# Kernel tuning notes

Measured on AMD Instinct MI355X. Metric: run time of the kernel, lower is better.

## Reference

```python
import jax, jax.numpy as jnp
import numpy as np

N = 50000
E = 800000
IN_CH = 256
HID = 32
HEADS = 4
OUT_CH = 40
NEG_SLOPE = 0.2
BN_EPS = 1e-5


def _gat_conv(x, W, att_src, att_dst, bias, src, dst, num_nodes, concat):
    # x: [N, F_in]; W: [F_in, H*C]; att_src/att_dst: [H, C]
    H, C = att_src.shape
    h = (x @ W).reshape(num_nodes, H, C)            # [N, H, C]
    a_src = (h * att_src[None]).sum(-1)             # [N, H]
    a_dst = (h * att_dst[None]).sum(-1)             # [N, H]
    e = jax.nn.leaky_relu(a_src[src] + a_dst[dst], NEG_SLOPE)  # [Etot, H]
    # segment softmax over incoming edges of each destination node
    m = jax.ops.segment_max(e, dst, num_segments=num_nodes)    # [N, H]
    ex = jnp.exp(e - m[dst])
    s = jax.ops.segment_sum(ex, dst, num_segments=num_nodes)   # [N, H]
    alpha = ex / (s[dst] + 1e-16)                   # [Etot, H]
    out = jax.ops.segment_sum(h[src] * alpha[:, :, None], dst,
                              num_segments=num_nodes)          # [N, H, C]
    out = out.reshape(num_nodes, H * C) if concat else out.mean(axis=1)
    return out + bias


def setup_inputs() -> dict:
    key = jax.random.key(0)
    ks = jax.random.split(key, 12)
    x = jax.random.normal(ks[0], (N, IN_CH), dtype=jnp.float32)
    edge_index = jax.random.randint(ks[1], (2, E), 0, N, dtype=jnp.int64)
    # layer 1: in -> heads*hid, concat
    W1 = jax.random.normal(ks[2], (IN_CH, HEADS * HID), dtype=jnp.float32) * (1.0 / np.sqrt(IN_CH))
    att_src1 = jax.random.normal(ks[3], (HEADS, HID), dtype=jnp.float32) * 0.1
    att_dst1 = jax.random.normal(ks[4], (HEADS, HID), dtype=jnp.float32) * 0.1
    b1 = jnp.zeros((HEADS * HID,), dtype=jnp.float32)
    # batch norm over hidden*heads features
    gamma = jnp.ones((HEADS * HID,), dtype=jnp.float32)
    beta = jnp.zeros((HEADS * HID,), dtype=jnp.float32)
    # layer 2: heads*hid -> out, heads=1, mean (concat=False)
    W2 = jax.random.normal(ks[5], (HEADS * HID, OUT_CH), dtype=jnp.float32) * (1.0 / np.sqrt(HEADS * HID))
    att_src2 = jax.random.normal(ks[6], (1, OUT_CH), dtype=jnp.float32) * 0.1
    att_dst2 = jax.random.normal(ks[7], (1, OUT_CH), dtype=jnp.float32) * 0.1
    b2 = jnp.zeros((OUT_CH,), dtype=jnp.float32)
    return {"x": x, "edge_index": edge_index, "W1": W1, "att_src1": att_src1,
            "att_dst1": att_dst1, "b1": b1, "gamma": gamma, "beta": beta,
            "W2": W2, "att_src2": att_src2, "att_dst2": att_dst2, "b2": b2}


def reference(x, edge_index, W1, att_src1, att_dst1, b1, gamma, beta,
              W2, att_src2, att_dst2, b2):
    num_nodes = x.shape[0]
    loops = jnp.arange(num_nodes, dtype=edge_index.dtype)
    src = jnp.concatenate([edge_index[0], loops])   # add self-loops (PyG default)
    dst = jnp.concatenate([edge_index[1], loops])
    h = _gat_conv(x, W1, att_src1, att_dst1, b1, src, dst, num_nodes, concat=True)
    # BatchNorm over nodes (training-mode batch statistics)
    mu = h.mean(axis=0)
    var = h.var(axis=0)
    h = (h - mu) * jax.lax.rsqrt(var + BN_EPS) * gamma + beta
    h = jax.nn.elu(h)
    out = _gat_conv(h, W2, att_src2, att_dst2, b2, src, dst, num_nodes, concat=False)
    return out
```

## Files before the change

### kernel.cpp

```cpp
#include <hip/hip_runtime.h>

#define NN 50000
#define EE 800000
#define ETOT 850000
#define FIN 256
#define F1 128
#define F2 40
#define CAP 48
#define G1B ((NN + 127) / 128)
#define FILLB ((EE / 4 + NN + 255) / 256)
#define PB ((NN + 63) / 64)

typedef unsigned int u32;
typedef unsigned short u16;

static __device__ __forceinline__ u32 f2bf(float f) {
  u32 u = __float_as_uint(f);
  return (u + 0x7FFFu + ((u >> 16) & 1u)) >> 16;
}
#define BF_LO(u) __uint_as_float((u) << 16)
#define BF_HI(u) __uint_as_float((u) & 0xFFFF0000u)

__global__ __launch_bounds__(256) void g1f_kernel(const float* __restrict__ x,
                                                  const float* __restrict__ W1,
                                                  const float* __restrict__ att_src,
                                                  const float* __restrict__ att_dst,
                                                  u32* __restrict__ h1bf,
                                                  float* __restrict__ a_src,
                                                  float* __restrict__ a_dst,
                                                  const int* __restrict__ ei,
                                                  int* __restrict__ cnt,
                                                  int* __restrict__ csr) {
  __shared__ float Alds[16 * 132];
  __shared__ float Blds[16 * 128];
  __shared__ float att_s[128], att_d[128];
  const int t = threadIdx.x;

  if (blockIdx.x >= G1B) {
    int i = (blockIdx.x - G1B) * 256 + t;
    if (i < EE / 4) {
      int e = i * 4;
      int4 s4 = *(const int4*)(ei + e);
      int4 d4 = *(const int4*)(ei + EE + e);
      int p0 = atomicAdd(cnt + d4.x, 1); if (p0 < CAP) csr[d4.x * CAP + p0] = s4.x;
      int p1 = atomicAdd(cnt + d4.y, 1); if (p1 < CAP) csr[d4.y * CAP + p1] = s4.y;
      int p2 = atomicAdd(cnt + d4.z, 1); if (p2 < CAP) csr[d4.z * CAP + p2] = s4.z;
      int p3 = atomicAdd(cnt + d4.w, 1); if (p3 < CAP) csr[d4.w * CAP + p3] = s4.w;
    } else {
      int n = i - EE / 4;
      if (n < NN) {
        int p = atomicAdd(cnt + n, 1);
        if (p < CAP) csr[n * CAP + p] = n;
      }
    }
    return;
  }

  if (t < 128) { att_s[t] = att_src[t]; att_d[t] = att_dst[t]; }
  const int m0 = blockIdx.x * 128;
  const int arow = t >> 1;
  const int akk = (t & 1) * 8;
  const int brow = t >> 4;
  const int bc = (t & 15) * 8;
  const int ty = t >> 4;
  const int tx = t & 15;

  float acc[8][8];
#pragma unroll
  for (int i = 0; i < 8; ++i)
#pragma unroll
    for (int j = 0; j < 8; ++j) acc[i][j] = 0.f;

  for (int k0 = 0; k0 < FIN; k0 += 16) {
    float4 a0 = {0.f, 0.f, 0.f, 0.f}, a1 = {0.f, 0.f, 0.f, 0.f};
    int gr = m0 + arow;
    if (gr < NN) {
      a0 = *(const float4*)(x + (size_t)gr * FIN + k0 + akk);
      a1 = *(const float4*)(x + (size_t)gr * FIN + k0 + akk + 4);
    }
    float4 b0 = *(const float4*)(W1 + (size_t)(k0 + brow) * F1 + bc);
    float4 b1 = *(const float4*)(W1 + (size_t)(k0 + brow) * F1 + bc + 4);
    __syncthreads();
    Alds[(akk + 0) * 132 + arow] = a0.x;
    Alds[(akk + 1) * 132 + arow] = a0.y;
    Alds[(akk + 2) * 132 + arow] = a0.z;
    Alds[(akk + 3) * 132 + arow] = a0.w;
    Alds[(akk + 4) * 132 + arow] = a1.x;
    Alds[(akk + 5) * 132 + arow] = a1.y;
    Alds[(akk + 6) * 132 + arow] = a1.z;
    Alds[(akk + 7) * 132 + arow] = a1.w;
    *(float4*)(Blds + brow * 128 + bc) = b0;
    *(float4*)(Blds + brow * 128 + bc + 4) = b1;
    __syncthreads();
#pragma unroll
    for (int k = 0; k < 16; ++k) {
      float4 av0 = *(const float4*)(Alds + k * 132 + ty * 8);
      float4 av1 = *(const float4*)(Alds + k * 132 + ty * 8 + 4);
      float4 bv0 = *(const float4*)(Blds + k * 128 + tx * 8);
      float4 bv1 = *(const float4*)(Blds + k * 128 + tx * 8 + 4);
      float aa[8] = {av0.x, av0.y, av0.z, av0.w, av1.x, av1.y, av1.z, av1.w};
      float bb[8] = {bv0.x, bv0.y, bv0.z, bv0.w, bv1.x, bv1.y, bv1.z, bv1.w};
#pragma unroll
      for (int i = 0; i < 8; ++i)
#pragma unroll
        for (int j = 0; j < 8; ++j) acc[i][j] = fmaf(aa[i], bb[j], acc[i][j]);
    }
  }
#pragma unroll
  for (int i = 0; i < 8; ++i) {
    int gr = m0 + ty * 8 + i;
    if (gr < NN) {
      uint4 w;
      w.x = f2bf(acc[i][0]) | (f2bf(acc[i][1]) << 16);
      w.y = f2bf(acc[i][2]) | (f2bf(acc[i][3]) << 16);
      w.z = f2bf(acc[i][4]) | (f2bf(acc[i][5]) << 16);
      w.w = f2bf(acc[i][6]) | (f2bf(acc[i][7]) << 16);
      *(uint4*)(h1bf + (size_t)gr * 64 + tx * 4) = w;
    }
  }
#pragma unroll
  for (int i = 0; i < 8; ++i) {
    float ps = 0.f, pd = 0.f;
#pragma unroll
    for (int j = 0; j < 8; ++j) {
      int c = tx * 8 + j;
      ps += acc[i][j] * att_s[c];
      pd += acc[i][j] * att_d[c];
    }
    ps += __shfl_xor(ps, 1); pd += __shfl_xor(pd, 1);
    ps += __shfl_xor(ps, 2); pd += __shfl_xor(pd, 2);
    if ((tx & 3) == 0) {
      int gr = m0 + ty * 8 + i;
      if (gr < NN) {
        int head = tx >> 2;
        a_src[gr * 4 + head] = ps;
        a_dst[gr * 4 + head] = pd;
      }
    }
  }
}

__global__ __launch_bounds__(256) void gather1_kernel(const int* __restrict__ cnt,
                                                      const int* __restrict__ csr,
                                                      const float* __restrict__ a_src,
                                                      const float* __restrict__ a_dst,
                                                      const u32* __restrict__ h1bf,
                                                      const float* __restrict__ b1,
                                                      float* __restrict__ h1b,
                                                      float* __restrict__ bnsum,
                                                      float* __restrict__ bnsq) {
  __shared__ float bns[32], bnq[32];
  int t = threadIdx.x;
  if (t < 32) { bns[t] = 0.f; bnq[t] = 0.f; }
  __syncthreads();
  int p = blockIdx.x / PB;
  int nb = blockIdx.x - p * PB;
  int n = nb * 64 + (t >> 2);
  int l = t & 3;
  int f0 = p * 32 + l * 8;
  if (n < NN) {
    float adst = a_dst[n * 4 + p];
    float acc[8] = {0.f, 0.f, 0.f, 0.f, 0.f, 0.f, 0.f, 0.f};
    float ssum = 0.f;
    const int* row = csr + n * CAP;
    int m = cnt[n]; if (m > CAP) m = CAP;
    const u32* hb = h1bf + p * 16 + l * 4;
    int i = 0;
    for (; i + 3 < m; i += 4) {
      int4 s4 = *(const int4*)(row + i);
      float e0 = a_src[s4.x * 4 + p] + adst;
      float e1 = a_src[s4.y * 4 + p] + adst;
      float e2 = a_src[s4.z * 4 + p] + adst;
      float e3 = a_src[s4.w * 4 + p] + adst;
      uint4 q0 = *(const uint4*)(hb + (size_t)s4.x * 64);
      uint4 q1 = *(const uint4*)(hb + (size_t)s4.y * 64);
      uint4 q2 = *(const uint4*)(hb + (size_t)s4.z * 64);
      uint4 q3 = *(const uint4*)(hb + (size_t)s4.w * 64);
      e0 = e0 > 0.f ? e0 : 0.2f * e0;  float x0 = __expf(e0);
      e1 = e1 > 0.f ? e1 : 0.2f * e1;  float x1 = __expf(e1);
      e2 = e2 > 0.f ? e2 : 0.2f * e2;  float x2 = __expf(e2);
      e3 = e3 > 0.f ? e3 : 0.2f * e3;  float x3 = __expf(e3);
      acc[0] = fmaf(x0, BF_LO(q0.x), acc[0]); acc[1] = fmaf(x0, BF_HI(q0.x), acc[1]);
      acc[2] = fmaf(x0, BF_LO(q0.y), acc[2]); acc[3] = fmaf(x0, BF_HI(q0.y), acc[3]);
      acc[4] = fmaf(x0, BF_LO(q0.z), acc[4]); acc[5] = fmaf(x0, BF_HI(q0.z), acc[5]);
      acc[6] = fmaf(x0, BF_LO(q0.w), acc[6]); acc[7] = fmaf(x0, BF_HI(q0.w), acc[7]);
      acc[0] = fmaf(x1, BF_LO(q1.x), acc[0]); acc[1] = fmaf(x1, BF_HI(q1.x), acc[1]);
      acc[2] = fmaf(x1, BF_LO(q1.y), acc[2]); acc[3] = fmaf(x1, BF_HI(q1.y), acc[3]);
      acc[4] = fmaf(x1, BF_LO(q1.z), acc[4]); acc[5] = fmaf(x1, BF_HI(q1.z), acc[5]);
      acc[6] = fmaf(x1, BF_LO(q1.w), acc[6]); acc[7] = fmaf(x1, BF_HI(q1.w), acc[7]);
      acc[0] = fmaf(x2, BF_LO(q2.x), acc[0]); acc[1] = fmaf(x2, BF_HI(q2.x), acc[1]);
      acc[2] = fmaf(x2, BF_LO(q2.y), acc[2]); acc[3] = fmaf(x2, BF_HI(q2.y), acc[3]);
      acc[4] = fmaf(x2, BF_LO(q2.z), acc[4]); acc[5] = fmaf(x2, BF_HI(q2.z), acc[5]);
      acc[6] = fmaf(x2, BF_LO(q2.w), acc[6]); acc[7] = fmaf(x2, BF_HI(q2.w), acc[7]);
      acc[0] = fmaf(x3, BF_LO(q3.x), acc[0]); acc[1] = fmaf(x3, BF_HI(q3.x), acc[1]);
      acc[2] = fmaf(x3, BF_LO(q3.y), acc[2]); acc[3] = fmaf(x3, BF_HI(q3.y), acc[3]);
      acc[4] = fmaf(x3, BF_LO(q3.z), acc[4]); acc[5] = fmaf(x3, BF_HI(q3.z), acc[5]);
      acc[6] = fmaf(x3, BF_LO(q3.w), acc[6]); acc[7] = fmaf(x3, BF_HI(q3.w), acc[7]);
      ssum += x0 + x1 + x2 + x3;
    }
    for (; i < m; ++i) {
      int s0 = row[i];
      float e0 = a_src[s0 * 4 + p] + adst;
      e0 = e0 > 0.f ? e0 : 0.2f * e0;
      float x0 = __expf(e0);
      uint4 q = *(const uint4*)(hb + (size_t)s0 * 64);
      acc[0] = fmaf(x0, BF_LO(q.x), acc[0]); acc[1] = fmaf(x0, BF_HI(q.x), acc[1]);
      acc[2] = fmaf(x0, BF_LO(q.y), acc[2]); acc[3] = fmaf(x0, BF_HI(q.y), acc[3]);
      acc[4] = fmaf(x0, BF_LO(q.z), acc[4]); acc[5] = fmaf(x0, BF_HI(q.z), acc[5]);
      acc[6] = fmaf(x0, BF_LO(q.w), acc[6]); acc[7] = fmaf(x0, BF_HI(q.w), acc[7]);
      ssum += x0;
    }
    float inv = 1.f / (ssum + 1e-16f);
    float4 b0 = *(const float4*)(b1 + f0);
    float4 b4 = *(const float4*)(b1 + f0 + 4);
    float o[8];
    o[0] = acc[0] * inv + b0.x; o[1] = acc[1] * inv + b0.y;
    o[2] = acc[2] * inv + b0.z; o[3] = acc[3] * inv + b0.w;
    o[4] = acc[4] * inv + b4.x; o[5] = acc[5] * inv + b4.y;
    o[6] = acc[6] * inv + b4.z; o[7] = acc[7] * inv + b4.w;
    float4 w0 = {o[0], o[1], o[2], o[3]};
    float4 w1 = {o[4], o[5], o[6], o[7]};
    *(float4*)(h1b + (size_t)n * F1 + f0) = w0;
    *(float4*)(h1b + (size_t)n * F1 + f0 + 4) = w1;
    int lb = l * 8;
#pragma unroll
    for (int j = 0; j < 8; ++j) {
      atomicAdd(&bns[lb + j], o[j]);
      atomicAdd(&bnq[lb + j], o[j] * o[j]);
    }
  }
  __syncthreads();
  if (t < 32) {
    atomicAdd(bnsum + p * 32 + t, bns[t]);
    atomicAdd(bnsq + p * 32 + t, bnq[t]);
  }
}

__global__ __launch_bounds__(256) void gemm2_kernel(const float* __restrict__ hpre,
                                                    const float* __restrict__ W2,
                                                    const float* __restrict__ bnsum,
                                                    const float* __restrict__ bnsq,
                                                    const float* __restrict__ gamma,
                                                    const float* __restrict__ beta,
                                                    const float* __restrict__ att_src2,
                                                    const float* __restrict__ att_dst2,
                                                    u16* __restrict__ h2bf,
                                                    float* __restrict__ a_src2,
                                                    float* __restrict__ a_dst2) {
  __shared__ float Wlds[128 * 40];
  __shared__ float Alds[16 * 128];
  __shared__ float sc[128], sh[128];
  int t = threadIdx.x;
  for (int i = t; i < 128 * 40; i += 256) Wlds[i] = W2[i];
  if (t < 128) {
    const float invN = 1.f / (float)NN;
    float mu = bnsum[t] * invN;
    float var = bnsq[t] * invN - mu * mu;
    float s = gamma[t] * rsqrtf(var + 1e-5f);
    sc[t] = s;
    sh[t] = beta[t] - mu * s;
  }
  int tr = t >> 3;
  int tc = t & 7;
  float as5[5], ad5[5];
#pragma unroll
  for (int j = 0; j < 5; ++j) { as5[j] = att_src2[tc * 5 + j]; ad5[j] = att_dst2[tc * 5 + j]; }
  int n0 = blockIdx.x * 128;
  int lrow = t >> 1;
  int lkk = (t & 1) * 8;
  float acc[4][5];
#pragma unroll
  for (int i = 0; i < 4; ++i)
#pragma unroll
    for (int j = 0; j < 5; ++j) acc[i][j] = 0.f;

  for (int k0 = 0; k0 < F1; k0 += 16) {
    float av[8];
    int gn = n0 + lrow;
    if (gn < NN) {
      float4 v0 = *(const float4*)(hpre + (size_t)gn * F1 + k0 + lkk);
      float4 v1 = *(const float4*)(hpre + (size_t)gn * F1 + k0 + lkk + 4);
      av[0] = v0.x; av[1] = v0.y; av[2] = v0.z; av[3] = v0.w;
      av[4] = v1.x; av[5] = v1.y; av[6] = v1.z; av[7] = v1.w;
    } else {
#pragma unroll
      for (int j = 0; j < 8; ++j) av[j] = 0.f;
    }
    __syncthreads();
#pragma unroll
    for (int j = 0; j < 8; ++j) {
      int kg = k0 + lkk + j;
      float a = av[j] * sc[kg] + sh[kg];
      a = a > 0.f ? a : (__expf(a) - 1.f);
      Alds[(lkk + j) * 128 + lrow] = a;
    }
    __syncthreads();
#pragma unroll
    for (int k = 0; k < 16; ++k) {
      float4 a4 = *(const float4*)(Alds + k * 128 + tr * 4);
      float aa[4] = {a4.x, a4.y, a4.z, a4.w};
      float w[5];
#pragma unroll
      for (int j = 0; j < 5; ++j) w[j] = Wlds[(k0 + k) * 40 + tc * 5 + j];
#pragma unroll
      for (int i = 0; i < 4; ++i)
#pragma unroll
        for (int j = 0; j < 5; ++j) acc[i][j] = fmaf(aa[i], w[j], acc[i][j]);
    }
  }
#pragma unroll
  for (int i = 0; i < 4; ++i) {
    int gn = n0 + tr * 4 + i;
    if (gn < NN) {
#pragma unroll
      for (int j = 0; j < 5; ++j)
        h2bf[(size_t)gn * 40 + tc * 5 + j] = (u16)f2bf(acc[i][j]);
    }
  }
#pragma unroll
  for (int i = 0; i < 4; ++i) {
    float ps = 0.f, pd = 0.f;
#pragma unroll
    for (int j = 0; j < 5; ++j) { ps += acc[i][j] * as5[j]; pd += acc[i][j] * ad5[j]; }
#pragma unroll
    for (int off = 1; off < 8; off <<= 1) {
      ps += __shfl_xor(ps, off);
      pd += __shfl_xor(pd, off);
    }
    if (tc == 0) {
      int gn = n0 + tr * 4 + i;
      if (gn < NN) { a_src2[gn] = ps; a_dst2[gn] = pd; }
    }
  }
}

__global__ __launch_bounds__(256) void gather2_kernel(const int* __restrict__ cnt,
                                                      const int* __restrict__ csr,
                                                      const float* __restrict__ a_src,
                                                      const float* __restrict__ a_dst,
                                                      const u32* __restrict__ h2bf,
                                                      const float* __restrict__ b2,
                                                      float* __restrict__ out) {
  int t = threadIdx.x;
  int n = blockIdx.x * 32 + (t >> 3);
  if (n >= NN) return;
  int l = t & 7;
  bool act = (l < 5);
  float adst = a_dst[n];
  float acc[8] = {0.f, 0.f, 0.f, 0.f, 0.f, 0.f, 0.f, 0.f};
  float ssum = 0.f;
  const int* row = csr + n * CAP;
  int m = cnt[n]; if (m > CAP) m = CAP;
  const uint4 zz = {0u, 0u, 0u, 0u};
  int i = 0;
  for (; i + 3 < m; i += 4) {
    int4 s4 = *(const int4*)(row + i);
    float e0 = a_src[s4.x] + adst;
    float e1 = a_src[s4.y] + adst;
    float e2 = a_src[s4.z] + adst;
    float e3 = a_src[s4.w] + adst;
    uint4 q0 = act ? *(const uint4*)(h2bf + (size_t)s4.x * 20 + l * 4) : zz;
    uint4 q1 = act ? *(const uint4*)(h2bf + (size_t)s4.y * 20 + l * 4) : zz;
    uint4 q2 = act ? *(const uint4*)(h2bf + (size_t)s4.z * 20 + l * 4) : zz;
    uint4 q3 = act ? *(const uint4*)(h2bf + (size_t)s4.w * 20 + l * 4) : zz;
    e0 = e0 > 0.f ? e0 : 0.2f * e0;  float x0 = __expf(e0);
    e1 = e1 > 0.f ? e1 : 0.2f * e1;  float x1 = __expf(e1);
    e2 = e2 > 0.f ? e2 : 0.2f * e2;  float x2 = __expf(e2);
    e3 = e3 > 0.f ? e3 : 0.2f * e3;  float x3 = __expf(e3);
    acc[0] = fmaf(x0, BF_LO(q0.x), acc[0]); acc[1] = fmaf(x0, BF_HI(q0.x), acc[1]);
    acc[2] = fmaf(x0, BF_LO(q0.y), acc[2]); acc[3] = fmaf(x0, BF_HI(q0.y), acc[3]);
    acc[4] = fmaf(x0, BF_LO(q0.z), acc[4]); acc[5] = fmaf(x0, BF_HI(q0.z), acc[5]);
    acc[6] = fmaf(x0, BF_LO(q0.w), acc[6]); acc[7] = fmaf(x0, BF_HI(q0.w), acc[7]);
    acc[0] = fmaf(x1, BF_LO(q1.x), acc[0]); acc[1] = fmaf(x1, BF_HI(q1.x), acc[1]);
    acc[2] = fmaf(x1, BF_LO(q1.y), acc[2]); acc[3] = fmaf(x1, BF_HI(q1.y), acc[3]);
    acc[4] = fmaf(x1, BF_LO(q1.z), acc[4]); acc[5] = fmaf(x1, BF_HI(q1.z), acc[5]);
    acc[6] = fmaf(x1, BF_LO(q1.w), acc[6]); acc[7] = fmaf(x1, BF_HI(q1.w), acc[7]);
    acc[0] = fmaf(x2, BF_LO(q2.x), acc[0]); acc[1] = fmaf(x2, BF_HI(q2.x), acc[1]);
    acc[2] = fmaf(x2, BF_LO(q2.y), acc[2]); acc[3] = fmaf(x2, BF_HI(q2.y), acc[3]);
    acc[4] = fmaf(x2, BF_LO(q2.z), acc[4]); acc[5] = fmaf(x2, BF_HI(q2.z), acc[5]);
    acc[6] = fmaf(x2, BF_LO(q2.w), acc[6]); acc[7] = fmaf(x2, BF_HI(q2.w), acc[7]);
    acc[0] = fmaf(x3, BF_LO(q3.x), acc[0]); acc[1] = fmaf(x3, BF_HI(q3.x), acc[1]);
    acc[2] = fmaf(x3, BF_LO(q3.y), acc[2]); acc[3] = fmaf(x3, BF_HI(q3.y), acc[3]);
    acc[4] = fmaf(x3, BF_LO(q3.z), acc[4]); acc[5] = fmaf(x3, BF_HI(q3.z), acc[5]);
    acc[6] = fmaf(x3, BF_LO(q3.w), acc[6]); acc[7] = fmaf(x3, BF_HI(q3.w), acc[7]);
    ssum += x0 + x1 + x2 + x3;
  }
  for (; i < m; ++i) {
    int s0 = row[i];
    float e0 = a_src[s0] + adst;
    e0 = e0 > 0.f ? e0 : 0.2f * e0;
    float x0 = __expf(e0);
    uint4 q = act ? *(const uint4*)(h2bf + (size_t)s0 * 20 + l * 4) : zz;
    acc[0] = fmaf(x0, BF_LO(q.x), acc[0]); acc[1] = fmaf(x0, BF_HI(q.x), acc[1]);
    acc[2] = fmaf(x0, BF_LO(q.y), acc[2]); acc[3] = fmaf(x0, BF_HI(q.y), acc[3]);
    acc[4] = fmaf(x0, BF_LO(q.z), acc[4]); acc[5] = fmaf(x0, BF_HI(q.z), acc[5]);
    acc[6] = fmaf(x0, BF_LO(q.w), acc[6]); acc[7] = fmaf(x0, BF_HI(q.w), acc[7]);
    ssum += x0;
  }
  float inv = 1.f / (ssum + 1e-16f);
  if (act) {
    float* op = out + (size_t)n * F2 + l * 8;
#pragma unroll
    for (int j = 0; j < 8; ++j) op[j] = acc[j] * inv + b2[l * 8 + j];
  }
}

extern "C" void kernel_launch(void* const* d_in, const int* in_sizes, int n_in,
                              void* d_out, int out_size, void* d_ws, size_t ws_size,
                              hipStream_t stream) {
  const float* x        = (const float*)d_in[0];
  const int*   ei       = (const int*)d_in[1];
  const float* W1       = (const float*)d_in[2];
  const float* att_src1 = (const float*)d_in[3];
  const float* att_dst1 = (const float*)d_in[4];
  const float* b1       = (const float*)d_in[5];
  const float* gamma    = (const float*)d_in[6];
  const float* beta     = (const float*)d_in[7];
  const float* W2       = (const float*)d_in[8];
  const float* att_src2 = (const float*)d_in[9];
  const float* att_dst2 = (const float*)d_in[10];
  const float* b2       = (const float*)d_in[11];
  float* out = (float*)d_out;

  int* cnt      = (int*)d_ws;
  float* bnsum  = (float*)(cnt + 50048);
  float* bnsq   = bnsum + 128;
  int* csr      = (int*)(bnsq + 128);
  u32* h1bf     = (u32*)(csr + NN * CAP);
  float* h1b    = (float*)(h1bf + 3200000);
  u32* h2bf     = (u32*)(h1b + 6400000);
  float* a_src1 = (float*)(h2bf + 1000000);
  float* a_dst1 = a_src1 + 200000;
  float* a_src2 = a_dst1 + 200000;
  float* a_dst2 = a_src2 + 50000;

  hipMemsetAsync(cnt, 0, (50048 + 256) * sizeof(int), stream);

  g1f_kernel<<<G1B + FILLB, 256, 0, stream>>>(x, W1, att_src1, att_dst1,
                                              h1bf, a_src1, a_dst1,
                                              ei, cnt, csr);
  gather1_kernel<<<4 * PB, 256, 0, stream>>>(cnt, csr, a_src1, a_dst1,
                                             h1bf, b1, h1b, bnsum, bnsq);
  gemm2_kernel<<<(NN + 127) / 128, 256, 0, stream>>>(h1b, W2, bnsum, bnsq,
                                                     gamma, beta,
                                                     att_src2, att_dst2,
                                                     (u16*)h2bf, a_src2, a_dst2);
  gather2_kernel<<<(NN + 31) / 32, 256, 0, stream>>>(cnt, csr, a_src2, a_dst2,
                                                     h2bf, b2, out);
}
```

Measured before the change: 323.8 us.

## Handle self-loops inline in gathers and split layer-2 features into aligned arrays

Self-loop edges are no longer written into the CSR by the fill blocks. Each gather kernel now adds the node's own contribution directly before walking its neighbour list, which removes N atomics and CSR writes and reads. The fill path goes back to one edge per thread with scalar loads instead of int4 vector loads. Layer-2 bf16 features, 80-byte rows before, are split into a 64-byte array and a 16-byte array so each gathered row is cache-line friendly, at the cost of two scattered loads per neighbour and a branchy store pattern in gemm2.

```diff
diff --git a/kernel.cpp b/kernel.cpp
--- a/kernel.cpp
+++ b/kernel.cpp
@@ -2,13 +2,12 @@
 
 #define NN 50000
 #define EE 800000
-#define ETOT 850000
 #define FIN 256
 #define F1 128
 #define F2 40
 #define CAP 48
 #define G1B ((NN + 127) / 128)
-#define FILLB ((EE / 4 + NN + 255) / 256)
+#define FILLB ((EE + 255) / 256)
 #define PB ((NN + 63) / 64)
 
 typedef unsigned int u32;
@@ -37,21 +36,12 @@
   const int t = threadIdx.x;
 
   if (blockIdx.x >= G1B) {
-    int i = (blockIdx.x - G1B) * 256 + t;
-    if (i < EE / 4) {
-      int e = i * 4;
-      int4 s4 = *(const int4*)(ei + e);
-      int4 d4 = *(const int4*)(ei + EE + e);
-      int p0 = atomicAdd(cnt + d4.x, 1); if (p0 < CAP) csr[d4.x * CAP + p0] = s4.x;
-      int p1 = atomicAdd(cnt + d4.y, 1); if (p1 < CAP) csr[d4.y * CAP + p1] = s4.y;
-      int p2 = atomicAdd(cnt + d4.z, 1); if (p2 < CAP) csr[d4.z * CAP + p2] = s4.z;
-      int p3 = atomicAdd(cnt + d4.w, 1); if (p3 < CAP) csr[d4.w * CAP + p3] = s4.w;
-    } else {
-      int n = i - EE / 4;
-      if (n < NN) {
-        int p = atomicAdd(cnt + n, 1);
-        if (p < CAP) csr[n * CAP + p] = n;
-      }
+    int e = (blockIdx.x - G1B) * 256 + t;
+    if (e < EE) {
+      int src = ei[e];
+      int dst = ei[EE + e];
+      int p = atomicAdd(cnt + dst, 1);
+      if (p < CAP) csr[dst * CAP + p] = src;
     }
     return;
   }
@@ -162,9 +152,20 @@
     float adst = a_dst[n * 4 + p];
     float acc[8] = {0.f, 0.f, 0.f, 0.f, 0.f, 0.f, 0.f, 0.f};
     float ssum = 0.f;
+    const u32* hb = h1bf + p * 16 + l * 4;
+    {
+      float e0 = a_src[n * 4 + p] + adst;
+      e0 = e0 > 0.f ? e0 : 0.2f * e0;
+      float x0 = __expf(e0);
+      uint4 q = *(const uint4*)(hb + (size_t)n * 64);
+      acc[0] = fmaf(x0, BF_LO(q.x), acc[0]); acc[1] = fmaf(x0, BF_HI(q.x), acc[1]);
+      acc[2] = fmaf(x0, BF_LO(q.y), acc[2]); acc[3] = fmaf(x0, BF_HI(q.y), acc[3]);
+      acc[4] = fmaf(x0, BF_LO(q.z), acc[4]); acc[5] = fmaf(x0, BF_HI(q.z), acc[5]);
+      acc[6] = fmaf(x0, BF_LO(q.w), acc[6]); acc[7] = fmaf(x0, BF_HI(q.w), acc[7]);
+      ssum += x0;
+    }
     const int* row = csr + n * CAP;
     int m = cnt[n]; if (m > CAP) m = CAP;
-    const u32* hb = h1bf + p * 16 + l * 4;
     int i = 0;
     for (; i + 3 < m; i += 4) {
       int4 s4 = *(const int4*)(row + i);
@@ -242,9 +243,10 @@
                                                     const float* __restrict__ bnsq,
                                                     const float* __restrict__ gamma,
                                                     const float* __restrict__ beta,
+                                                    u16* __restrict__ h2a,
+                                                    u16* __restrict__ h2b,
                                                     const float* __restrict__ att_src2,
                                                     const float* __restrict__ att_dst2,
-                                                    u16* __restrict__ h2bf,
                                                     float* __restrict__ a_src2,
                                                     float* __restrict__ a_dst2) {
   __shared__ float Wlds[128 * 40];
@@ -313,8 +315,12 @@
     int gn = n0 + tr * 4 + i;
     if (gn < NN) {
 #pragma unroll
-      for (int j = 0; j < 5; ++j)
-        h2bf[(size_t)gn * 40 + tc * 5 + j] = (u16)f2bf(acc[i][j]);
+      for (int j = 0; j < 5; ++j) {
+        int f = tc * 5 + j;
+        u16 v = (u16)f2bf(acc[i][j]);
+        if (f < 32) h2a[(size_t)gn * 32 + f] = v;
+        else        h2b[(size_t)gn * 8 + (f - 32)] = v;
+      }
     }
   }
 #pragma unroll
@@ -338,7 +344,8 @@
                                                       const int* __restrict__ csr,
                                                       const float* __restrict__ a_src,
                                                       const float* __restrict__ a_dst,
-                                                      const u32* __restrict__ h2bf,
+                                                      const u32* __restrict__ h2a,
+                                                      const u32* __restrict__ h2b,
                                                       const float* __restrict__ b2,
                                                       float* __restrict__ out) {
   int t = threadIdx.x;
@@ -346,12 +353,25 @@
   if (n >= NN) return;
   int l = t & 7;
   bool act = (l < 5);
+  bool isA = (l < 4);
   float adst = a_dst[n];
   float acc[8] = {0.f, 0.f, 0.f, 0.f, 0.f, 0.f, 0.f, 0.f};
   float ssum = 0.f;
+  const uint4 zz = {0u, 0u, 0u, 0u};
+  {
+    float e0 = a_src[n] + adst;
+    e0 = e0 > 0.f ? e0 : 0.2f * e0;
+    float x0 = __expf(e0);
+    uint4 q = act ? (isA ? *(const uint4*)(h2a + (size_t)n * 16 + l * 4)
+                         : *(const uint4*)(h2b + (size_t)n * 4)) : zz;
+    acc[0] = fmaf(x0, BF_LO(q.x), acc[0]); acc[1] = fmaf(x0, BF_HI(q.x), acc[1]);
+    acc[2] = fmaf(x0, BF_LO(q.y), acc[2]); acc[3] = fmaf(x0, BF_HI(q.y), acc[3]);
+    acc[4] = fmaf(x0, BF_LO(q.z), acc[4]); acc[5] = fmaf(x0, BF_HI(q.z), acc[5]);
+    acc[6] = fmaf(x0, BF_LO(q.w), acc[6]); acc[7] = fmaf(x0, BF_HI(q.w), acc[7]);
+    ssum += x0;
+  }
   const int* row = csr + n * CAP;
   int m = cnt[n]; if (m > CAP) m = CAP;
-  const uint4 zz = {0u, 0u, 0u, 0u};
   int i = 0;
   for (; i + 3 < m; i += 4) {
     int4 s4 = *(const int4*)(row + i);
@@ -359,10 +379,14 @@
     float e1 = a_src[s4.y] + adst;
     float e2 = a_src[s4.z] + adst;
     float e3 = a_src[s4.w] + adst;
-    uint4 q0 = act ? *(const uint4*)(h2bf + (size_t)s4.x * 20 + l * 4) : zz;
-    uint4 q1 = act ? *(const uint4*)(h2bf + (size_t)s4.y * 20 + l * 4) : zz;
-    uint4 q2 = act ? *(const uint4*)(h2bf + (size_t)s4.z * 20 + l * 4) : zz;
-    uint4 q3 = act ? *(const uint4*)(h2bf + (size_t)s4.w * 20 + l * 4) : zz;
+    uint4 q0 = act ? (isA ? *(const uint4*)(h2a + (size_t)s4.x * 16 + l * 4)
+                          : *(const uint4*)(h2b + (size_t)s4.x * 4)) : zz;
+    uint4 q1 = act ? (isA ? *(const uint4*)(h2a + (size_t)s4.y * 16 + l * 4)
+                          : *(const uint4*)(h2b + (size_t)s4.y * 4)) : zz;
+    uint4 q2 = act ? (isA ? *(const uint4*)(h2a + (size_t)s4.z * 16 + l * 4)
+                          : *(const uint4*)(h2b + (size_t)s4.z * 4)) : zz;
+    uint4 q3 = act ? (isA ? *(const uint4*)(h2a + (size_t)s4.w * 16 + l * 4)
+                          : *(const uint4*)(h2b + (size_t)s4.w * 4)) : zz;
     e0 = e0 > 0.f ? e0 : 0.2f * e0;  float x0 = __expf(e0);
     e1 = e1 > 0.f ? e1 : 0.2f * e1;  float x1 = __expf(e1);
     e2 = e2 > 0.f ? e2 : 0.2f * e2;  float x2 = __expf(e2);
@@ -390,7 +414,8 @@
     float e0 = a_src[s0] + adst;
     e0 = e0 > 0.f ? e0 : 0.2f * e0;
     float x0 = __expf(e0);
-    uint4 q = act ? *(const uint4*)(h2bf + (size_t)s0 * 20 + l * 4) : zz;
+    uint4 q = act ? (isA ? *(const uint4*)(h2a + (size_t)s0 * 16 + l * 4)
+                         : *(const uint4*)(h2b + (size_t)s0 * 4)) : zz;
     acc[0] = fmaf(x0, BF_LO(q.x), acc[0]); acc[1] = fmaf(x0, BF_HI(q.x), acc[1]);
     acc[2] = fmaf(x0, BF_LO(q.y), acc[2]); acc[3] = fmaf(x0, BF_HI(q.y), acc[3]);
     acc[4] = fmaf(x0, BF_LO(q.z), acc[4]); acc[5] = fmaf(x0, BF_HI(q.z), acc[5]);
@@ -428,8 +453,9 @@
   int* csr      = (int*)(bnsq + 128);
   u32* h1bf     = (u32*)(csr + NN * CAP);
   float* h1b    = (float*)(h1bf + 3200000);
-  u32* h2bf     = (u32*)(h1b + 6400000);
-  float* a_src1 = (float*)(h2bf + 1000000);
+  u32* h2a      = (u32*)(h1b + 6400000);
+  u32* h2b      = h2a + 800000;
+  float* a_src1 = (float*)(h2b + 200000);
   float* a_dst1 = a_src1 + 200000;
   float* a_src2 = a_dst1 + 200000;
   float* a_dst2 = a_src2 + 50000;
@@ -443,8 +469,9 @@
                                              h1bf, b1, h1b, bnsum, bnsq);
   gemm2_kernel<<<(NN + 127) / 128, 256, 0, stream>>>(h1b, W2, bnsum, bnsq,
                                                      gamma, beta,
+                                                     (u16*)h2a, (u16*)h2b,
                                                      att_src2, att_dst2,
-                                                     (u16*)h2bf, a_src2, a_dst2);
+                                                     a_src2, a_dst2);
   gather2_kernel<<<(NN + 31) / 32, 256, 0, stream>>>(cnt, csr, a_src2, a_dst2,
-                                                     h2bf, b2, out);
-}
+                                                     h2a, h2b, b2, out);
+}
```

Measured after the change: 323.4 us. Within noise of the previous version (-0.1%).
